# Optimization experiments

Hardware: AMD Instinct MI355X
Metric: run time of the kernel (lower is better)

Reference implementation:

```python
import jax, jax.numpy as jnp
import numpy as np

EMBED_DIM = 1024
NUM_HEADS = 16
HEAD_DIM = EMBED_DIM // NUM_HEADS
MAX_REL = 64
B, S = 4, 1024


def setup_inputs() -> dict:
    key = jax.random.key(0)
    ks = jax.random.split(key, 12)
    scale = 1.0 / np.sqrt(EMBED_DIM)
    inp = {
        "query": jax.random.normal(ks[0], (B, S, EMBED_DIM), jnp.float32),
        "key": jax.random.normal(ks[1], (B, S, EMBED_DIM), jnp.float32),
        "value": jax.random.normal(ks[2], (B, S, EMBED_DIM), jnp.float32),
        "attn_mask": jnp.ones((B, 1, S, S), jnp.int32),
        # projection weights stored [in, out] so x @ W matches torch Linear(x) with W = weight.T
        "Wq": jax.random.normal(ks[3], (EMBED_DIM, EMBED_DIM), jnp.float32) * scale,
        "bq": jnp.zeros((EMBED_DIM,), jnp.float32),
        "Wk": jax.random.normal(ks[4], (EMBED_DIM, EMBED_DIM), jnp.float32) * scale,
        "bk": jnp.zeros((EMBED_DIM,), jnp.float32),
        "Wv": jax.random.normal(ks[5], (EMBED_DIM, EMBED_DIM), jnp.float32) * scale,
        "bv": jnp.zeros((EMBED_DIM,), jnp.float32),
        "Wo": jax.random.normal(ks[6], (EMBED_DIM, EMBED_DIM), jnp.float32) * scale,
        "bo": jnp.zeros((EMBED_DIM,), jnp.float32),
        "rel_pos_embed": jax.random.normal(ks[7], (2 * MAX_REL + 1, HEAD_DIM), jnp.float32) * 0.02,
    }
    return inp


def _split_heads(x):
    # [B, S, E] -> [B, H, S, D]
    b, s, _ = x.shape
    return x.reshape(b, s, NUM_HEADS, HEAD_DIM).transpose(0, 2, 1, 3)


def reference(query, key, value, attn_mask, Wq, bq, Wk, bk, Wv, bv, Wo, bo, rel_pos_embed):
    q = _split_heads(query @ Wq + bq)
    k = _split_heads(key @ Wk + bk)
    v = _split_heads(value @ Wv + bv)

    scores = jnp.einsum("bhqd,bhkd->bhqk", q, k) / np.sqrt(HEAD_DIM).astype(np.float32)

    # relative position bias: rel_pos[i, j] = rel_pos_embed[clip(i - j) + MAX_REL]
    seq_len = scores.shape[-1]
    rng = jnp.arange(seq_len)
    range_mat = jnp.clip(rng[:, None] - rng[None, :], -MAX_REL, MAX_REL) + MAX_REL
    rel_pos = rel_pos_embed[range_mat]                       # [S, S, D]
    # torch: matmul(q[...,None,:], rel_pos.mT).squeeze(-2) == einsum over head_dim (NOT scaled)
    rel_scores = jnp.einsum("bhid,ijd->bhij", q, rel_pos)
    scores = scores + rel_scores

    scores = jnp.where(attn_mask == 0, -jnp.inf, scores)
    attn_weights = jax.nn.softmax(scores, axis=-1)           # dropout p=0.0 -> identity

    out = jnp.einsum("bhqk,bhkd->bhqd", attn_weights, v)
    out = out.transpose(0, 2, 1, 3).reshape(query.shape[0], -1, EMBED_DIM)
    out = out @ Wo + bo
    return out, attn_weights
```

## Files before the change

kernel.cpp:

```cpp
#include <hip/hip_runtime.h>
#include <math.h>

#define BB 4
#define SS 1024
#define EE 1024
#define HH 16
#define DD 64
#define RR 129
#define PRELW 130

typedef __attribute__((ext_vector_type(4))) float f32x4;
typedef __attribute__((ext_vector_type(8))) short bf8;
typedef __attribute__((ext_vector_type(4))) short s4v;

#define MFMA(a, b, c) __builtin_amdgcn_mfma_f32_16x16x32_bf16(a, b, c, 0, 0, 0)

__device__ __forceinline__ float bf2f(unsigned short u) {
    return __uint_as_float(((unsigned)u) << 16);
}
__device__ __forceinline__ unsigned short f2bf(float x) {
    unsigned u = __float_as_uint(x);
    return (unsigned short)((u + 0x7fffu + ((u >> 16) & 1u)) >> 16);
}

__global__ __launch_bounds__(256, 4)
void wtrans_kernel(const float* __restrict__ Wq, const float* __restrict__ Wk,
                   const float* __restrict__ Wv, const float* __restrict__ Wo,
                   unsigned short* __restrict__ wt_hi, unsigned short* __restrict__ wt_lo)
{
    __shared__ float T[64][65];
    const int w = blockIdx.z;
    const float* W = w == 0 ? Wq : (w == 1 ? Wk : (w == 2 ? Wv : Wo));
    const int n0 = blockIdx.x * 64, k0 = blockIdx.y * 64;
    const int tid = threadIdx.x;
#pragma unroll
    for (int i = 0; i < 4; ++i) {
        int c = tid + 256 * i; int r = c >> 4, c4 = c & 15;
        f32x4 v = *(const f32x4*)(W + (size_t)(k0 + r) * EE + n0 + c4 * 4);
        T[r][c4 * 4 + 0] = v.x; T[r][c4 * 4 + 1] = v.y;
        T[r][c4 * 4 + 2] = v.z; T[r][c4 * 4 + 3] = v.w;
    }
    __syncthreads();
#pragma unroll
    for (int i = 0; i < 4; ++i) {
        int c = tid + 256 * i; int r = c >> 4, c4 = c & 15;
        float x0 = T[c4 * 4 + 0][r], x1 = T[c4 * 4 + 1][r];
        float x2 = T[c4 * 4 + 2][r], x3 = T[c4 * 4 + 3][r];
        unsigned short h0 = f2bf(x0), h1 = f2bf(x1), h2 = f2bf(x2), h3 = f2bf(x3);
        unsigned short l0 = f2bf(x0 - bf2f(h0)), l1 = f2bf(x1 - bf2f(h1));
        unsigned short l2 = f2bf(x2 - bf2f(h2)), l3 = f2bf(x3 - bf2f(h3));
        size_t o = (size_t)w * 1048576 + (size_t)(n0 + r) * 1024 + k0 + c4 * 4;
        *(s4v*)&wt_hi[o] = (s4v){(short)h0, (short)h1, (short)h2, (short)h3};
        *(s4v*)&wt_lo[o] = (s4v){(short)l0, (short)l1, (short)l2, (short)l3};
    }
}

__global__ __launch_bounds__(256)
void maskbits_kernel(const int* __restrict__ mask, unsigned long long* __restrict__ mb)
{
    const int w = blockIdx.x * 256 + threadIdx.x;
    const int* p = mask + (size_t)w * 64;
    unsigned long long bits = 0;
#pragma unroll
    for (int i = 0; i < 16; ++i) {
        int4 v = *(const int4*)(p + i * 4);
        bits |= (unsigned long long)(v.x != 0) << (i * 4 + 0);
        bits |= (unsigned long long)(v.y != 0) << (i * 4 + 1);
        bits |= (unsigned long long)(v.z != 0) << (i * 4 + 2);
        bits |= (unsigned long long)(v.w != 0) << (i * 4 + 3);
    }
    mb[w] = bits;
}

template<int ASRC, int EPI>
__device__ __forceinline__ void gemm_body(
    const float* __restrict__ Af,
    const unsigned short* __restrict__ Ah_g, const unsigned short* __restrict__ Al_g,
    const unsigned short* __restrict__ Bh_g, const unsigned short* __restrict__ Bl_g,
    const float* __restrict__ bias,
    float* __restrict__ Yf, unsigned short* __restrict__ Yh, unsigned short* __restrict__ Yl,
    unsigned short* As_h, unsigned short* As_l, unsigned short* Bs_h, unsigned short* Bs_l,
    int m0, int n0)
{
    const int tid = threadIdx.x, lane = tid & 63, wid = tid >> 6;
    const int wm = (wid >> 1) * 64, wn = (wid & 1) * 64;
    f32x4 zero4 = {0.f, 0.f, 0.f, 0.f};
    f32x4 acc[4][4];
#pragma unroll
    for (int a = 0; a < 4; ++a)
#pragma unroll
        for (int b = 0; b < 4; ++b) acc[a][b] = zero4;

    for (int kt = 0; kt < 1024; kt += 64) {
        __syncthreads();
        if (ASRC == 0) {
#pragma unroll
            for (int i = 0; i < 8; ++i) {
                int c = tid + 256 * i; int r = c >> 4, c4 = c & 15;
                f32x4 v = *(const f32x4*)(Af + (size_t)(m0 + r) * 1024 + kt + c4 * 4);
                unsigned short h0 = f2bf(v.x), h1 = f2bf(v.y), h2 = f2bf(v.z), h3 = f2bf(v.w);
                unsigned short l0 = f2bf(v.x - bf2f(h0)), l1 = f2bf(v.y - bf2f(h1));
                unsigned short l2 = f2bf(v.z - bf2f(h2)), l3 = f2bf(v.w - bf2f(h3));
                int off = r * 64 + (((c4 >> 1) ^ (r & 7)) * 8) + (c4 & 1) * 4;
                *(s4v*)&As_h[off] = (s4v){(short)h0, (short)h1, (short)h2, (short)h3};
                *(s4v*)&As_l[off] = (s4v){(short)l0, (short)l1, (short)l2, (short)l3};
            }
        } else {
#pragma unroll
            for (int i = 0; i < 4; ++i) {
                int c = tid + 256 * i; int r = c >> 3, cc = c & 7;
                int off = r * 64 + ((cc ^ (r & 7)) * 8);
                *(bf8*)&As_h[off] = *(const bf8*)(Ah_g + (size_t)(m0 + r) * 1024 + kt + cc * 8);
                *(bf8*)&As_l[off] = *(const bf8*)(Al_g + (size_t)(m0 + r) * 1024 + kt + cc * 8);
            }
        }
#pragma unroll
        for (int i = 0; i < 4; ++i) {
            int c = tid + 256 * i; int r = c >> 3, cc = c & 7;
            int off = r * 64 + ((cc ^ (r & 7)) * 8);
            *(bf8*)&Bs_h[off] = *(const bf8*)(Bh_g + (size_t)(n0 + r) * 1024 + kt + cc * 8);
            *(bf8*)&Bs_l[off] = *(const bf8*)(Bl_g + (size_t)(n0 + r) * 1024 + kt + cc * 8);
        }
        __syncthreads();
#pragma unroll
        for (int ks = 0; ks < 2; ++ks) {
            bf8 ah[4], al[4], bh[4], bl[4];
#pragma unroll
            for (int f = 0; f < 4; ++f) {
                int ra = wm + f * 16 + (lane & 15);
                int ca = (ks * 4 + (lane >> 4)) ^ (ra & 7);
                ah[f] = *(const bf8*)&As_h[ra * 64 + ca * 8];
                al[f] = *(const bf8*)&As_l[ra * 64 + ca * 8];
                int rb = wn + f * 16 + (lane & 15);
                int cb = (ks * 4 + (lane >> 4)) ^ (rb & 7);
                bh[f] = *(const bf8*)&Bs_h[rb * 64 + cb * 8];
                bl[f] = *(const bf8*)&Bs_l[rb * 64 + cb * 8];
            }
#pragma unroll
            for (int fi = 0; fi < 4; ++fi)
#pragma unroll
                for (int fj = 0; fj < 4; ++fj) {
                    acc[fi][fj] = MFMA(ah[fi], bh[fj], acc[fi][fj]);
                    acc[fi][fj] = MFMA(al[fi], bh[fj], acc[fi][fj]);
                    acc[fi][fj] = MFMA(ah[fi], bl[fj], acc[fi][fj]);
                }
        }
    }
#pragma unroll
    for (int fi = 0; fi < 4; ++fi)
#pragma unroll
        for (int fj = 0; fj < 4; ++fj)
#pragma unroll
            for (int rg = 0; rg < 4; ++rg) {
                int m = m0 + wm + fi * 16 + ((lane >> 4) << 2) + rg;
                int n = n0 + wn + fj * 16 + (lane & 15);
                float val = acc[fi][fj][rg] + bias[n];
                if (EPI == 0) {
                    int b = m >> 10, s = m & 1023, h = n >> 6, d = n & 63;
                    size_t o = (((size_t)(b * 16 + h)) * 1024 + s) * 64 + d;
                    unsigned short hv = f2bf(val);
                    unsigned short lv = f2bf(val - bf2f(hv));
                    Yh[o] = hv; Yl[o] = lv;
                } else {
                    Yf[(size_t)m * 1024 + n] = val;
                }
            }
}

__global__ __launch_bounds__(256, 2)
void proj_qkv_kernel(const float* __restrict__ q_in, const float* __restrict__ k_in,
                     const float* __restrict__ v_in,
                     const unsigned short* __restrict__ wt_hi, const unsigned short* __restrict__ wt_lo,
                     const float* __restrict__ bq, const float* __restrict__ bk,
                     const float* __restrict__ bv,
                     unsigned short* qh_hi, unsigned short* qh_lo,
                     unsigned short* kh_hi, unsigned short* kh_lo,
                     unsigned short* vh_hi, unsigned short* vh_lo)
{
    __shared__ __align__(16) unsigned short As_h[128 * 64], As_l[128 * 64];
    __shared__ __align__(16) unsigned short Bs_h[128 * 64], Bs_l[128 * 64];
    const int z = blockIdx.z;
    const float* X = z == 0 ? q_in : (z == 1 ? k_in : v_in);
    const float* bias = z == 0 ? bq : (z == 1 ? bk : bv);
    unsigned short* Yh = z == 0 ? qh_hi : (z == 1 ? kh_hi : vh_hi);
    unsigned short* Yl = z == 0 ? qh_lo : (z == 1 ? kh_lo : vh_lo);
    gemm_body<0, 0>(X, nullptr, nullptr,
                    wt_hi + (size_t)z * 1048576, wt_lo + (size_t)z * 1048576,
                    bias, nullptr, Yh, Yl, As_h, As_l, Bs_h, Bs_l,
                    blockIdx.x * 128, blockIdx.y * 128);
}

__global__ __launch_bounds__(256, 2)
void outproj_kernel(const unsigned short* __restrict__ ctx_hi, const unsigned short* __restrict__ ctx_lo,
                    const unsigned short* __restrict__ wo_hi, const unsigned short* __restrict__ wo_lo,
                    const float* __restrict__ bo, float* __restrict__ out)
{
    __shared__ __align__(16) unsigned short As_h[128 * 64], As_l[128 * 64];
    __shared__ __align__(16) unsigned short Bs_h[128 * 64], Bs_l[128 * 64];
    gemm_body<1, 1>(nullptr, ctx_hi, ctx_lo, wo_hi, wo_lo, bo, out, nullptr, nullptr,
                    As_h, As_l, Bs_h, Bs_l, blockIdx.x * 128, blockIdx.y * 128);
}

__global__ __launch_bounds__(256, 4)
void vtrans_kernel(const unsigned short* __restrict__ vh_hi, const unsigned short* __restrict__ vh_lo,
                   unsigned short* __restrict__ vt_hi, unsigned short* __restrict__ vt_lo)
{
    __shared__ unsigned short T[64][72];
    const unsigned short* src = blockIdx.z ? vh_lo : vh_hi;
    unsigned short* dst = blockIdx.z ? vt_lo : vt_hi;
    const int st = blockIdx.x * 64, bh = blockIdx.y, tid = threadIdx.x;
#pragma unroll
    for (int i = 0; i < 4; ++i) {
        int c = tid + 256 * i; int r = c >> 4, d4 = c & 15;
        s4v v = *(const s4v*)(src + ((size_t)bh * 1024 + st + r) * 64 + d4 * 4);
        T[r][d4 * 4 + 0] = (unsigned short)v.x; T[r][d4 * 4 + 1] = (unsigned short)v.y;
        T[r][d4 * 4 + 2] = (unsigned short)v.z; T[r][d4 * 4 + 3] = (unsigned short)v.w;
    }
    __syncthreads();
#pragma unroll
    for (int i = 0; i < 4; ++i) {
        int c = tid + 256 * i; int r = c >> 4, s4_ = c & 15;
        s4v o = {(short)T[s4_ * 4 + 0][r], (short)T[s4_ * 4 + 1][r],
                 (short)T[s4_ * 4 + 2][r], (short)T[s4_ * 4 + 3][r]};
        *(s4v*)(dst + ((size_t)bh * 64 + r) * 1024 + st + s4_ * 4) = o;
    }
}

__global__ __launch_bounds__(256, 2)
void relproj_kernel(const unsigned short* __restrict__ qh_hi, const float* __restrict__ emb,
                    unsigned short* __restrict__ prel)
{
    __shared__ float se[RR][68];
    __shared__ float sq[128][68];
    const int tid = threadIdx.x;
    const size_t row0 = (size_t)blockIdx.x * 128;
    for (int i = tid; i < RR * 64; i += 256) { int r = i >> 6, d = i & 63; se[r][d] = emb[i]; }
#pragma unroll
    for (int i = 0; i < 8; ++i) {
        int c = tid + 256 * i; int r = c >> 4, d4 = c & 15;
        s4v v = *(const s4v*)(qh_hi + (row0 + r) * 64 + d4 * 4);
        sq[r][d4 * 4 + 0] = bf2f((unsigned short)v.x);
        sq[r][d4 * 4 + 1] = bf2f((unsigned short)v.y);
        sq[r][d4 * 4 + 2] = bf2f((unsigned short)v.z);
        sq[r][d4 * 4 + 3] = bf2f((unsigned short)v.w);
    }
    __syncthreads();
    for (int idx = tid; idx < 128 * RR; idx += 256) {
        int r = idx / RR, c = idx - r * RR;
        const float* a = sq[r];
        const float* b = se[c];
        float s = 0.f;
#pragma unroll
        for (int d = 0; d < 64; ++d) s = fmaf(a[d], b[d], s);
        prel[(row0 + r) * PRELW + c] = f2bf(s);
    }
}

__global__ __launch_bounds__(256, 2)
void scores_kernel(const unsigned short* __restrict__ qh_hi, const unsigned short* __restrict__ qh_lo,
                   const unsigned short* __restrict__ kh_hi, const unsigned short* __restrict__ kh_lo,
                   const unsigned short* __restrict__ prel, const unsigned long long* __restrict__ mb,
                   float* __restrict__ attn, float* __restrict__ rowm, float* __restrict__ rowsum)
{
    __shared__ __align__(16) unsigned short Sh[128 * 64], Sl[128 * 64];
    __shared__ __align__(16) unsigned short Pr[128 * PRELW];
    __shared__ float Sm[2][128], Ss[2][128];
    const int tid = threadIdx.x, lane = tid & 63, wid = tid >> 6;
    const int wi = wid >> 1, wj = wid & 1;
    const int g = lane >> 4, li = lane & 15;
    const int i0 = blockIdx.x * 128, bh = blockIdx.y, b = bh >> 4;

    const unsigned short* qbh = qh_hi + ((size_t)bh * 1024 + i0) * 64;
    const unsigned short* qbl = qh_lo + ((size_t)bh * 1024 + i0) * 64;
#pragma unroll
    for (int i = 0; i < 4; ++i) {
        int c = tid + 256 * i; int r = c >> 3, cc = c & 7;
        int off = r * 64 + ((cc ^ (r & 7)) * 8);
        *(bf8*)&Sh[off] = *(const bf8*)(qbh + r * 64 + cc * 8);
        *(bf8*)&Sl[off] = *(const bf8*)(qbl + r * 64 + cc * 8);
    }
    {
        const unsigned* src = (const unsigned*)(prel + ((size_t)bh * 1024 + i0) * PRELW);
        unsigned* dst = (unsigned*)Pr;
        for (int idx = tid; idx < 128 * (PRELW / 2); idx += 256) dst[idx] = src[idx];
    }
    __syncthreads();
    bf8 qfh[4][2], qfl[4][2];
#pragma unroll
    for (int fi = 0; fi < 4; ++fi)
#pragma unroll
        for (int ks = 0; ks < 2; ++ks) {
            int rb = wi * 64 + fi * 16 + li;
            int cb = (ks * 4 + g) ^ (rb & 7);
            qfh[fi][ks] = *(const bf8*)&Sh[rb * 64 + cb * 8];
            qfl[fi][ks] = *(const bf8*)&Sl[rb * 64 + cb * 8];
        }

    float rm[4], rs[4];
#pragma unroll
    for (int i = 0; i < 4; ++i) { rm[i] = -3.0e38f; rs[i] = 0.f; }

    for (int jt = 0; jt < 8; ++jt) {
        __syncthreads();
        const unsigned short* kbh = kh_hi + ((size_t)bh * 1024 + jt * 128) * 64;
        const unsigned short* kbl = kh_lo + ((size_t)bh * 1024 + jt * 128) * 64;
#pragma unroll
        for (int i = 0; i < 4; ++i) {
            int c = tid + 256 * i; int r = c >> 3, cc = c & 7;
            int off = r * 64 + ((cc ^ (r & 7)) * 8);
            *(bf8*)&Sh[off] = *(const bf8*)(kbh + r * 64 + cc * 8);
            *(bf8*)&Sl[off] = *(const bf8*)(kbl + r * 64 + cc * 8);
        }
        __syncthreads();
        f32x4 zero4 = {0.f, 0.f, 0.f, 0.f};
        f32x4 acc[4][4];
#pragma unroll
        for (int a = 0; a < 4; ++a)
#pragma unroll
            for (int c = 0; c < 4; ++c) acc[a][c] = zero4;
#pragma unroll
        for (int ks = 0; ks < 2; ++ks) {
            bf8 kfh[4], kfl[4];
#pragma unroll
            for (int fj = 0; fj < 4; ++fj) {
                int ra = wj * 64 + fj * 16 + li;
                int ca = (ks * 4 + g) ^ (ra & 7);
                kfh[fj] = *(const bf8*)&Sh[ra * 64 + ca * 8];
                kfl[fj] = *(const bf8*)&Sl[ra * 64 + ca * 8];
            }
#pragma unroll
            for (int fj = 0; fj < 4; ++fj)
#pragma unroll
                for (int fi = 0; fi < 4; ++fi) {
                    acc[fj][fi] = MFMA(kfh[fj], qfh[fi][ks], acc[fj][fi]);
                    acc[fj][fi] = MFMA(kfl[fj], qfh[fi][ks], acc[fj][fi]);
                    acc[fj][fi] = MFMA(kfh[fj], qfl[fi][ks], acc[fj][fi]);
                }
        }
#pragma unroll
        for (int fi = 0; fi < 4; ++fi) {
            const int rowL = wi * 64 + fi * 16 + li;
            const int ii = i0 + rowL;
            const unsigned long long mw = mb[((size_t)b * 1024 + ii) * 16 + jt * 2 + wj];
            float p16[4][4];
            float tmax = -3.0e38f;
#pragma unroll
            for (int fj = 0; fj < 4; ++fj)
#pragma unroll
                for (int rg = 0; rg < 4; ++rg) {
                    int jloc = fj * 16 + g * 4 + rg;
                    int jj = jt * 128 + wj * 64 + jloc;
                    int dd = ii - jj; dd = dd < -64 ? -64 : (dd > 64 ? 64 : dd);
                    float s = acc[fj][fi][rg] * 0.125f + bf2f(Pr[rowL * PRELW + dd + 64]);
                    if (!((mw >> jloc) & 1ull)) s = -1.0e30f;
                    p16[fj][rg] = s;
                    tmax = fmaxf(tmax, s);
                }
            tmax = fmaxf(tmax, __shfl_xor(tmax, 16, 64));
            tmax = fmaxf(tmax, __shfl_xor(tmax, 32, 64));
            float nm = fmaxf(rm[fi], tmax);
            float ps = 0.f;
#pragma unroll
            for (int fj = 0; fj < 4; ++fj)
#pragma unroll
                for (int rg = 0; rg < 4; ++rg) ps += __expf(p16[fj][rg] - nm);
            ps += __shfl_xor(ps, 16, 64);
            ps += __shfl_xor(ps, 32, 64);
            rs[fi] = rs[fi] * __expf(rm[fi] - nm) + ps;
            rm[fi] = nm;
            float* arow = attn + ((size_t)bh * 1024 + ii) * 1024 + jt * 128 + wj * 64 + g * 4;
#pragma unroll
            for (int fj = 0; fj < 4; ++fj) {
                f32x4 st = {p16[fj][0], p16[fj][1], p16[fj][2], p16[fj][3]};
                *(f32x4*)(arow + fj * 16) = st;
            }
        }
    }
#pragma unroll
    for (int fi = 0; fi < 4; ++fi) {
        if (lane < 16) {
            Sm[wj][wi * 64 + fi * 16 + li] = rm[fi];
            Ss[wj][wi * 64 + fi * 16 + li] = rs[fi];
        }
    }
    __syncthreads();
    if (tid < 128) {
        float m0_ = Sm[0][tid], m1_ = Sm[1][tid];
        float mm = fmaxf(m0_, m1_);
        float ss = Ss[0][tid] * __expf(m0_ - mm) + Ss[1][tid] * __expf(m1_ - mm);
        rowm[(size_t)bh * 1024 + i0 + tid] = mm;
        rowsum[(size_t)bh * 1024 + i0 + tid] = ss;
    }
}

__global__ __launch_bounds__(256, 2)
void pv_kernel(float* __restrict__ attn,
               const unsigned short* __restrict__ vt_hi, const unsigned short* __restrict__ vt_lo,
               const float* __restrict__ rowm, const float* __restrict__ rowsum,
               unsigned short* __restrict__ ctx_hi, unsigned short* __restrict__ ctx_lo)
{
    const int tid = threadIdx.x, lane = tid & 63, wid = tid >> 6;
    const int g = lane >> 4, li = lane & 15;
    const int i0 = blockIdx.x * 128, bh = blockIdx.y;

    float mmv[2], ivv[2];
    float* arow[2];
#pragma unroll
    for (int fi = 0; fi < 2; ++fi) {
        const int rr = wid * 32 + fi * 16 + li;
        mmv[fi] = rowm[(size_t)bh * 1024 + i0 + rr];
        ivv[fi] = 1.f / rowsum[(size_t)bh * 1024 + i0 + rr];
        arow[fi] = attn + ((size_t)bh * 1024 + i0 + rr) * 1024 + g * 8;
    }
    const unsigned short* vbh = vt_hi + (size_t)bh * 65536 + (size_t)li * 1024 + g * 8;
    const unsigned short* vbl = vt_lo + (size_t)bh * 65536 + (size_t)li * 1024 + g * 8;

    f32x4 zero4 = {0.f, 0.f, 0.f, 0.f};
    f32x4 acc[2][4];
#pragma unroll
    for (int a = 0; a < 2; ++a)
#pragma unroll
        for (int c = 0; c < 4; ++c) acc[a][c] = zero4;

    for (int jc = 0; jc < 32; ++jc) {
        bf8 ah[2], al[2];
#pragma unroll
        for (int fi = 0; fi < 2; ++fi) {
            float* ap = arow[fi] + jc * 32;
            f32x4 v0 = *(const f32x4*)ap;
            f32x4 v1 = *(const f32x4*)(ap + 4);
            const float mm = mmv[fi], iv = ivv[fi];
            float p0 = __expf(v0.x - mm) * iv, p1 = __expf(v0.y - mm) * iv;
            float p2 = __expf(v0.z - mm) * iv, p3 = __expf(v0.w - mm) * iv;
            float p4 = __expf(v1.x - mm) * iv, p5 = __expf(v1.y - mm) * iv;
            float p6 = __expf(v1.z - mm) * iv, p7 = __expf(v1.w - mm) * iv;
            f32x4 o0 = {p0, p1, p2, p3}, o1 = {p4, p5, p6, p7};
            *(f32x4*)ap = o0;
            *(f32x4*)(ap + 4) = o1;
            unsigned short h0 = f2bf(p0), h1 = f2bf(p1), h2 = f2bf(p2), h3 = f2bf(p3);
            unsigned short h4 = f2bf(p4), h5 = f2bf(p5), h6 = f2bf(p6), h7 = f2bf(p7);
            ah[fi] = (bf8){(short)h0, (short)h1, (short)h2, (short)h3,
                           (short)h4, (short)h5, (short)h6, (short)h7};
            al[fi] = (bf8){(short)f2bf(p0 - bf2f(h0)), (short)f2bf(p1 - bf2f(h1)),
                           (short)f2bf(p2 - bf2f(h2)), (short)f2bf(p3 - bf2f(h3)),
                           (short)f2bf(p4 - bf2f(h4)), (short)f2bf(p5 - bf2f(h5)),
                           (short)f2bf(p6 - bf2f(h6)), (short)f2bf(p7 - bf2f(h7))};
        }
#pragma unroll
        for (int fj = 0; fj < 4; ++fj) {
            bf8 bh_ = *(const bf8*)(vbh + (size_t)fj * 16384 + jc * 32);
            bf8 bl_ = *(const bf8*)(vbl + (size_t)fj * 16384 + jc * 32);
#pragma unroll
            for (int fi = 0; fi < 2; ++fi) {
                acc[fi][fj] = MFMA(ah[fi], bh_, acc[fi][fj]);
                acc[fi][fj] = MFMA(al[fi], bh_, acc[fi][fj]);
                acc[fi][fj] = MFMA(ah[fi], bl_, acc[fi][fj]);
            }
        }
    }
    const int b = bh >> 4, h = bh & 15;
#pragma unroll
    for (int fi = 0; fi < 2; ++fi)
#pragma unroll
        for (int fj = 0; fj < 4; ++fj)
#pragma unroll
            for (int rg = 0; rg < 4; ++rg) {
                int ii = i0 + wid * 32 + fi * 16 + g * 4 + rg;
                int d = fj * 16 + li;
                float val = acc[fi][fj][rg];
                size_t o = ((size_t)b * 1024 + ii) * 1024 + h * 64 + d;
                unsigned short hv = f2bf(val);
                unsigned short lv = f2bf(val - bf2f(hv));
                ctx_hi[o] = hv; ctx_lo[o] = lv;
            }
}

extern "C" void kernel_launch(void* const* d_in, const int* in_sizes, int n_in,
                              void* d_out, int out_size, void* d_ws, size_t ws_size,
                              hipStream_t stream)
{
    const float* query = (const float*)d_in[0];
    const float* key_  = (const float*)d_in[1];
    const float* value = (const float*)d_in[2];
    const int*   mask  = (const int*)d_in[3];
    const float* Wq = (const float*)d_in[4];
    const float* bq = (const float*)d_in[5];
    const float* Wk = (const float*)d_in[6];
    const float* bk = (const float*)d_in[7];
    const float* Wv = (const float*)d_in[8];
    const float* bv = (const float*)d_in[9];
    const float* Wo = (const float*)d_in[10];
    const float* bo = (const float*)d_in[11];
    const float* emb = (const float*)d_in[12];

    unsigned short* wt_hi = (unsigned short*)d_ws;
    unsigned short* wt_lo = wt_hi + (size_t)4 * 1048576;
    unsigned short* qh_hi = wt_lo + (size_t)4 * 1048576;
    unsigned short* qh_lo = qh_hi + 4194304;
    unsigned short* kh_hi = qh_lo + 4194304;
    unsigned short* kh_lo = kh_hi + 4194304;
    unsigned short* vt_hi = kh_lo + 4194304;
    unsigned short* vt_lo = vt_hi + 4194304;
    unsigned short* prel  = vt_lo + 4194304;
    float* rowm   = (float*)d_ws;
    float* rowsum = rowm + 65536;
    unsigned long long* mb = (unsigned long long*)(rowsum + 65536);
    unsigned short* ctx_hi = qh_hi;
    unsigned short* ctx_lo = qh_lo;
    unsigned short* vh_hi = (unsigned short*)d_out;
    unsigned short* vh_lo = vh_hi + 4194304;

    float* out  = (float*)d_out;
    float* attn = (float*)d_out + 4194304;

    dim3 blk(256);
    wtrans_kernel<<<dim3(16, 16, 4), blk, 0, stream>>>(Wq, Wk, Wv, Wo, wt_hi, wt_lo);
    proj_qkv_kernel<<<dim3(32, 8, 3), blk, 0, stream>>>(query, key_, value, wt_hi, wt_lo,
                                                        bq, bk, bv, qh_hi, qh_lo,
                                                        kh_hi, kh_lo, vh_hi, vh_lo);
    maskbits_kernel<<<dim3(256), blk, 0, stream>>>(mask, mb);
    vtrans_kernel<<<dim3(16, 64, 2), blk, 0, stream>>>(vh_hi, vh_lo, vt_hi, vt_lo);
    relproj_kernel<<<dim3(512), blk, 0, stream>>>(qh_hi, emb, prel);
    scores_kernel<<<dim3(8, 64), blk, 0, stream>>>(qh_hi, qh_lo, kh_hi, kh_lo, prel, mb,
                                                   attn, rowm, rowsum);
    pv_kernel<<<dim3(8, 64), blk, 0, stream>>>(attn, vt_hi, vt_lo, rowm, rowsum, ctx_hi, ctx_lo);
    outproj_kernel<<<dim3(32, 8), blk, 0, stream>>>(ctx_hi, ctx_lo,
                                                    wt_hi + (size_t)3 * 1048576,
                                                    wt_lo + (size_t)3 * 1048576, bo, out);
}
```

Measured before the change: 547.2 us.

## Shrink pv_kernel tile to 16 rows per wave and prefetch attention chunks

New measurement: 565.8 us. 1.03x slower.

```diff
diff --git a/kernel.cpp b/kernel.cpp
--- a/kernel.cpp
+++ b/kernel.cpp
@@ -393,7 +393,7 @@
     }
 }
 
-__global__ __launch_bounds__(256, 2)
+__global__ __launch_bounds__(256, 4)
 void pv_kernel(float* __restrict__ attn,
                const unsigned short* __restrict__ vt_hi, const unsigned short* __restrict__ vt_lo,
                const float* __restrict__ rowm, const float* __restrict__ rowsum,
@@ -401,78 +401,66 @@
 {
     const int tid = threadIdx.x, lane = tid & 63, wid = tid >> 6;
     const int g = lane >> 4, li = lane & 15;
-    const int i0 = blockIdx.x * 128, bh = blockIdx.y;
-
-    float mmv[2], ivv[2];
-    float* arow[2];
-#pragma unroll
-    for (int fi = 0; fi < 2; ++fi) {
-        const int rr = wid * 32 + fi * 16 + li;
-        mmv[fi] = rowm[(size_t)bh * 1024 + i0 + rr];
-        ivv[fi] = 1.f / rowsum[(size_t)bh * 1024 + i0 + rr];
-        arow[fi] = attn + ((size_t)bh * 1024 + i0 + rr) * 1024 + g * 8;
-    }
+    const int i0 = blockIdx.x * 64, bh = blockIdx.y;
+    const int row = i0 + wid * 16 + li;
+
+    const float mm = rowm[(size_t)bh * 1024 + row];
+    const float iv = 1.f / rowsum[(size_t)bh * 1024 + row];
+    float* ap = attn + ((size_t)bh * 1024 + row) * 1024 + g * 8;
     const unsigned short* vbh = vt_hi + (size_t)bh * 65536 + (size_t)li * 1024 + g * 8;
     const unsigned short* vbl = vt_lo + (size_t)bh * 65536 + (size_t)li * 1024 + g * 8;
 
     f32x4 zero4 = {0.f, 0.f, 0.f, 0.f};
-    f32x4 acc[2][4];
-#pragma unroll
-    for (int a = 0; a < 2; ++a)
-#pragma unroll
-        for (int c = 0; c < 4; ++c) acc[a][c] = zero4;
-
+    f32x4 acc[4] = {zero4, zero4, zero4, zero4};
+
+    f32x4 c0 = *(const f32x4*)ap;
+    f32x4 c1 = *(const f32x4*)(ap + 4);
     for (int jc = 0; jc < 32; ++jc) {
-        bf8 ah[2], al[2];
-#pragma unroll
-        for (int fi = 0; fi < 2; ++fi) {
-            float* ap = arow[fi] + jc * 32;
-            f32x4 v0 = *(const f32x4*)ap;
-            f32x4 v1 = *(const f32x4*)(ap + 4);
-            const float mm = mmv[fi], iv = ivv[fi];
-            float p0 = __expf(v0.x - mm) * iv, p1 = __expf(v0.y - mm) * iv;
-            float p2 = __expf(v0.z - mm) * iv, p3 = __expf(v0.w - mm) * iv;
-            float p4 = __expf(v1.x - mm) * iv, p5 = __expf(v1.y - mm) * iv;
-            float p6 = __expf(v1.z - mm) * iv, p7 = __expf(v1.w - mm) * iv;
-            f32x4 o0 = {p0, p1, p2, p3}, o1 = {p4, p5, p6, p7};
-            *(f32x4*)ap = o0;
-            *(f32x4*)(ap + 4) = o1;
-            unsigned short h0 = f2bf(p0), h1 = f2bf(p1), h2 = f2bf(p2), h3 = f2bf(p3);
-            unsigned short h4 = f2bf(p4), h5 = f2bf(p5), h6 = f2bf(p6), h7 = f2bf(p7);
-            ah[fi] = (bf8){(short)h0, (short)h1, (short)h2, (short)h3,
-                           (short)h4, (short)h5, (short)h6, (short)h7};
-            al[fi] = (bf8){(short)f2bf(p0 - bf2f(h0)), (short)f2bf(p1 - bf2f(h1)),
-                           (short)f2bf(p2 - bf2f(h2)), (short)f2bf(p3 - bf2f(h3)),
-                           (short)f2bf(p4 - bf2f(h4)), (short)f2bf(p5 - bf2f(h5)),
-                           (short)f2bf(p6 - bf2f(h6)), (short)f2bf(p7 - bf2f(h7))};
-        }
+        const int nidx = (jc < 31 ? jc + 1 : 0) * 32;
+        f32x4 n0 = *(const f32x4*)(ap + nidx);
+        f32x4 n1 = *(const f32x4*)(ap + nidx + 4);
+        bf8 vh_[4], vl_[4];
 #pragma unroll
         for (int fj = 0; fj < 4; ++fj) {
-            bf8 bh_ = *(const bf8*)(vbh + (size_t)fj * 16384 + jc * 32);
-            bf8 bl_ = *(const bf8*)(vbl + (size_t)fj * 16384 + jc * 32);
-#pragma unroll
-            for (int fi = 0; fi < 2; ++fi) {
-                acc[fi][fj] = MFMA(ah[fi], bh_, acc[fi][fj]);
-                acc[fi][fj] = MFMA(al[fi], bh_, acc[fi][fj]);
-                acc[fi][fj] = MFMA(ah[fi], bl_, acc[fi][fj]);
-            }
-        }
+            vh_[fj] = *(const bf8*)(vbh + (size_t)fj * 16384 + jc * 32);
+            vl_[fj] = *(const bf8*)(vbl + (size_t)fj * 16384 + jc * 32);
+        }
+        float p0 = __expf(c0.x - mm) * iv, p1 = __expf(c0.y - mm) * iv;
+        float p2 = __expf(c0.z - mm) * iv, p3 = __expf(c0.w - mm) * iv;
+        float p4 = __expf(c1.x - mm) * iv, p5 = __expf(c1.y - mm) * iv;
+        float p6 = __expf(c1.z - mm) * iv, p7 = __expf(c1.w - mm) * iv;
+        f32x4 o0 = {p0, p1, p2, p3}, o1 = {p4, p5, p6, p7};
+        *(f32x4*)(ap + jc * 32) = o0;
+        *(f32x4*)(ap + jc * 32 + 4) = o1;
+        unsigned short h0 = f2bf(p0), h1 = f2bf(p1), h2 = f2bf(p2), h3 = f2bf(p3);
+        unsigned short h4 = f2bf(p4), h5 = f2bf(p5), h6 = f2bf(p6), h7 = f2bf(p7);
+        bf8 ah = {(short)h0, (short)h1, (short)h2, (short)h3,
+                  (short)h4, (short)h5, (short)h6, (short)h7};
+        bf8 al = {(short)f2bf(p0 - bf2f(h0)), (short)f2bf(p1 - bf2f(h1)),
+                  (short)f2bf(p2 - bf2f(h2)), (short)f2bf(p3 - bf2f(h3)),
+                  (short)f2bf(p4 - bf2f(h4)), (short)f2bf(p5 - bf2f(h5)),
+                  (short)f2bf(p6 - bf2f(h6)), (short)f2bf(p7 - bf2f(h7))};
+#pragma unroll
+        for (int fj = 0; fj < 4; ++fj) {
+            acc[fj] = MFMA(ah, vh_[fj], acc[fj]);
+            acc[fj] = MFMA(al, vh_[fj], acc[fj]);
+            acc[fj] = MFMA(ah, vl_[fj], acc[fj]);
+        }
+        c0 = n0; c1 = n1;
     }
     const int b = bh >> 4, h = bh & 15;
 #pragma unroll
-    for (int fi = 0; fi < 2; ++fi)
-#pragma unroll
-        for (int fj = 0; fj < 4; ++fj)
-#pragma unroll
-            for (int rg = 0; rg < 4; ++rg) {
-                int ii = i0 + wid * 32 + fi * 16 + g * 4 + rg;
-                int d = fj * 16 + li;
-                float val = acc[fi][fj][rg];
-                size_t o = ((size_t)b * 1024 + ii) * 1024 + h * 64 + d;
-                unsigned short hv = f2bf(val);
-                unsigned short lv = f2bf(val - bf2f(hv));
-                ctx_hi[o] = hv; ctx_lo[o] = lv;
-            }
+    for (int fj = 0; fj < 4; ++fj)
+#pragma unroll
+        for (int rg = 0; rg < 4; ++rg) {
+            int ii = i0 + wid * 16 + g * 4 + rg;
+            int d = fj * 16 + li;
+            float val = acc[fj][rg];
+            size_t o = ((size_t)b * 1024 + ii) * 1024 + h * 64 + d;
+            unsigned short hv = f2bf(val);
+            unsigned short lv = f2bf(val - bf2f(hv));
+            ctx_hi[o] = hv; ctx_lo[o] = lv;
+        }
 }
 
 extern "C" void kernel_launch(void* const* d_in, const int* in_sizes, int n_in,
@@ -523,7 +511,7 @@
     relproj_kernel<<<dim3(512), blk, 0, stream>>>(qh_hi, emb, prel);
     scores_kernel<<<dim3(8, 64), blk, 0, stream>>>(qh_hi, qh_lo, kh_hi, kh_lo, prel, mb,
                                                    attn, rowm, rowsum);
-    pv_kernel<<<dim3(8, 64), blk, 0, stream>>>(attn, vt_hi, vt_lo, rowm, rowsum, ctx_hi, ctx_lo);
+    pv_kernel<<<dim3(16, 64), blk, 0, stream>>>(attn, vt_hi, vt_lo, rowm, rowsum, ctx_hi, ctx_lo);
     outproj_kernel<<<dim3(32, 8), blk, 0, stream>>>(ctx_hi, ctx_lo,
                                                     wt_hi + (size_t)3 * 1048576,
                                                     wt_lo + (size_t)3 * 1048576, bo, out);
```
